# Performance work log

Measured on AMD Instinct MI355X. Metric: run time of the kernel, lower is better.

The kernel has to match this reference:

```python
import jax, jax.numpy as jnp
import numpy as np

WZ, WH, WW = 2, 6, 12
WIN = WZ * WH * WW  # 144
DEPTH, DIM, HEADS = 2, 192, 6
NEG = -1e9


def earth_position_index():
    zi = np.arange(WZ); zj = -np.arange(WZ) * WZ
    hi = np.arange(WH); hj = -np.arange(WH) * WH
    w = np.arange(WW)
    c1 = np.stack(np.meshgrid(zi, hi, w, indexing='ij')).reshape(3, -1)
    c2 = np.stack(np.meshgrid(zj, hj, w, indexing='ij')).reshape(3, -1)
    coords = (c1[:, :, None] - c2[:, None, :]).transpose(1, 2, 0).copy()
    coords[:, :, 2] += WW - 1
    coords[:, :, 1] *= 2 * WW - 1
    coords[:, :, 0] *= (2 * WW - 1) * WH * WH
    return jnp.asarray(coords.sum(-1))


def shift_mask(Z, H):
    # Swin-style mask over Z (vertical) and H (latitude); W (longitude) is circular.
    sz, sh = WZ // 2, WH // 2
    region = np.zeros((Z, H), np.int32)
    cnt = 0
    for zs in (slice(0, Z - WZ), slice(Z - WZ, Z - sz), slice(Z - sz, Z)):
        for hs in (slice(0, H - WH), slice(H - WH, H - sh), slice(H - sh, H)):
            region[zs, hs] = cnt; cnt += 1
    r = region.reshape(Z // WZ, WZ, H // WH, WH).transpose(0, 2, 1, 3).reshape(-1, WZ * WH)
    r = np.repeat(r, WW, axis=1)  # window token order is (z,h,w)
    m = np.where(r[:, :, None] == r[:, None, :], 0.0, NEG).astype(np.float32)
    return jnp.asarray(m)


def window_partition(x, Z, H, W):
    B, C = x.shape[0], x.shape[-1]
    x = x.reshape(B, Z // WZ, WZ, H // WH, WH, W // WW, WW, C)
    x = x.transpose(0, 1, 3, 5, 2, 4, 6, 7)
    return x.reshape(B, (Z // WZ) * (H // WH) * (W // WW), WIN, C)


def window_reverse(xw, Z, H, W):
    B, C = xw.shape[0], xw.shape[-1]
    x = xw.reshape(B, Z // WZ, H // WH, W // WW, WZ, WH, WW, C)
    x = x.transpose(0, 1, 4, 2, 5, 3, 6, 7)
    return x.reshape(B, Z, H, W, C)


def layernorm(x, g, b):
    mu = x.mean(-1, keepdims=True)
    var = jnp.mean((x - mu) ** 2, axis=-1, keepdims=True)
    return (x - mu) * jax.lax.rsqrt(var + 1e-5) * g + b


def attn_windows(xw, qkv_w, qkv_b, proj_w, proj_b, bias_tab, pos_idx, mask):
    B, nW, N, C = xw.shape
    hd = C // HEADS
    qkv = (xw @ qkv_w + qkv_b).reshape(B, nW, N, 3, HEADS, hd)
    q, k, v = qkv[..., 0, :, :], qkv[..., 1, :, :], qkv[..., 2, :, :]
    attn = jnp.einsum('bwnhd,bwmhd->bwhnm', q * (hd ** -0.5), k)
    bias = bias_tab[pos_idx]
    attn = attn + bias.transpose(2, 0, 1)[None, None]
    if mask is not None:
        nzh = mask.shape[0]
        attn = attn.reshape(B, nzh, nW // nzh, HEADS, N, N) + mask[None, :, None, None]
        attn = attn.reshape(B, nW, HEADS, N, N)
    attn = jax.nn.softmax(attn, axis=-1)
    out = jnp.einsum('bwhnm,bwmhd->bwnhd', attn, v).reshape(B, nW, N, C)
    return out @ proj_w + proj_b


def forward(x, qkv_w, qkv_b, proj_w, proj_b, bias_tab,
            ln1_g, ln1_b, ln2_g, ln2_b, mlp_w1, mlp_b1, mlp_w2, mlp_b2, Z, H, W):
    B, L, C = x.shape
    pos_idx = earth_position_index()
    mask = shift_mask(Z, H)
    depth = qkv_w.shape[0]
    for i in range(depth):
        roll = (i % 2 == 1)
        shortcut = x
        xg = x.reshape(B, Z, H, W, C)
        if roll:
            xg = jnp.roll(xg, (-(WZ // 2), -(WH // 2), -(WW // 2)), axis=(1, 2, 3))
        xw = window_partition(xg, Z, H, W)
        xw = attn_windows(xw, qkv_w[i], qkv_b[i], proj_w[i], proj_b[i],
                          bias_tab[i], pos_idx, mask if roll else None)
        xg = window_reverse(xw, Z, H, W)
        if roll:
            xg = jnp.roll(xg, (WZ // 2, WH // 2, WW // 2), axis=(1, 2, 3))
        xa = xg.reshape(B, L, C)
        x = shortcut + layernorm(xa, ln1_g[i], ln1_b[i])
        h = jax.nn.gelu(x @ mlp_w1[i] + mlp_b1[i], approximate=False)
        h = h @ mlp_w2[i] + mlp_b2[i]
        x = x + layernorm(h, ln2_g[i], ln2_b[i])
    return x


def setup_inputs() -> dict:
    key = jax.random.key(0)
    ks = jax.random.split(key, 16)
    B, Z, H, W, C = 1, 8, 96, 180, DIM
    L = Z * H * W
    bias_rows = (2 * WW - 1) * WH * WH * WZ * WZ  # 3312
    s = 0.02
    return {
        'x': jax.random.normal(ks[0], (B, L, C), jnp.float32),
        'qkv_w': jax.random.normal(ks[1], (DEPTH, C, 3 * C), jnp.float32) * s,
        'qkv_b': jnp.zeros((DEPTH, 3 * C), jnp.float32),
        'proj_w': jax.random.normal(ks[2], (DEPTH, C, C), jnp.float32) * s,
        'proj_b': jnp.zeros((DEPTH, C), jnp.float32),
        'bias_tab': jax.random.normal(ks[3], (DEPTH, bias_rows, HEADS), jnp.float32) * s,
        'ln1_g': jnp.ones((DEPTH, C), jnp.float32),
        'ln1_b': jnp.zeros((DEPTH, C), jnp.float32),
        'ln2_g': jnp.ones((DEPTH, C), jnp.float32),
        'ln2_b': jnp.zeros((DEPTH, C), jnp.float32),
        'mlp_w1': jax.random.normal(ks[4], (DEPTH, C, 4 * C), jnp.float32) * s,
        'mlp_b1': jnp.zeros((DEPTH, 4 * C), jnp.float32),
        'mlp_w2': jax.random.normal(ks[5], (DEPTH, 4 * C, C), jnp.float32) * s,
        'mlp_b2': jnp.zeros((DEPTH, C), jnp.float32),
        'Z': Z, 'H': H, 'W': W,
    }


def reference(x, qkv_w, qkv_b, proj_w, proj_b, bias_tab, ln1_g, ln1_b, ln2_g, ln2_b,
              mlp_w1, mlp_b1, mlp_w2, mlp_b2, Z, H, W):
    return forward(x, qkv_w, qkv_b, proj_w, proj_b, bias_tab, ln1_g, ln1_b,
                   ln2_g, ln2_b, mlp_w1, mlp_b1, mlp_w2, mlp_b2, Z, H, W)
```

## Files before the change

kernel.cpp:

```cpp
#include <hip/hip_runtime.h>
#include <hip/hip_bf16.h>
#include <math.h>

#define L_TOK 138240
#define NW 960

typedef __attribute__((ext_vector_type(8))) short s16x8;
typedef __attribute__((ext_vector_type(8))) unsigned short u16x8;
typedef __attribute__((ext_vector_type(4))) unsigned short u16x4;
typedef __attribute__((ext_vector_type(4))) float f32x4;

__device__ __forceinline__ float bf2f(unsigned short u){
  union{unsigned int u;float f;} v; v.u=((unsigned int)u)<<16; return v.f;
}
__device__ __forceinline__ unsigned short f2bf(float f){
  __hip_bfloat16 b = __float2bfloat16(f);
  union { __hip_bfloat16 b; unsigned short u; } v; v.b = b; return v.u;
}
__device__ __forceinline__ void gll16(const void* g, void* l) {
  __builtin_amdgcn_global_load_lds((const __attribute__((address_space(1))) void*)g,
                                   (__attribute__((address_space(3))) void*)l, 16, 0, 0);
}
__device__ __forceinline__ float gelu_f(float v){
  const float s = v * 0.70710678118654752f;
  const float a = fabsf(s);
  const float t = 1.0f / (1.0f + 0.3275911f * a);
  float p = 1.061405429f;
  p = p*t - 1.453152027f;
  p = p*t + 1.421413741f;
  p = p*t - 0.284496736f;
  p = p*t + 0.254829592f;
  p = p*t;
  float y = 1.0f - p * __expf(-a*a);
  y = copysignf(y, s);
  return 0.5f * v * (1.0f + y);
}

template<int NTILES>
__global__ __launch_bounds__(256) void gemm_qkv(
    const unsigned short* __restrict__ xb,
    const unsigned short* __restrict__ Bt,
    const float* __restrict__ bias,
    unsigned short* __restrict__ out)
{
  __shared__ unsigned short As[64*192];
  const int tid = threadIdx.x;
  const int wid = tid >> 6, lane = tid & 63;
  const int lr = lane & 15, kg = lane >> 4;
  const int bm = blockIdx.x;
  const int wn = wid * 16;
  const int N = NTILES * 64;

  #pragma unroll
  for (int i = 0; i < 6; i++) {
    const int c = tid + i*256;
    const int r = c / 24, s = c % 24;
    const int sg = (s & 24) | ((s ^ r) & 7);
    gll16(&xb[(size_t)(bm*64 + r)*192 + sg*8], &As[c*8]);
  }
  __syncthreads();

  s16x8 a[4][6];
  #pragma unroll
  for (int mi = 0; mi < 4; mi++)
    #pragma unroll
    for (int ks = 0; ks < 6; ks++) {
      const int m = mi*16 + lr, g = ks*4 + kg;
      const int sg = (g & 24) | ((g ^ m) & 7);
      a[mi][ks] = *(const s16x8*)&As[m*192 + sg*8];
    }

  for (int bn = 0; bn < NTILES; bn++) {
    s16x8 b[6];
    #pragma unroll
    for (int ks = 0; ks < 6; ks++)
      b[ks] = *(const s16x8*)&Bt[(size_t)(bn*64 + wn + lr)*192 + ks*32 + kg*8];
    f32x4 acc[4] = {};
    #pragma unroll
    for (int ks = 0; ks < 6; ks++)
      #pragma unroll
      for (int mi = 0; mi < 4; mi++)
        acc[mi] = __builtin_amdgcn_mfma_f32_16x16x32_bf16(a[mi][ks], b[ks], acc[mi], 0, 0, 0);
    const int col = bn*64 + wn + lr;
    const float bv = bias[col];
    #pragma unroll
    for (int mi = 0; mi < 4; mi++)
      #pragma unroll
      for (int q = 0; q < 4; q++) {
        const int row = bm*64 + mi*16 + kg*4 + q;
        out[(size_t)row*N + col] = f2bf(acc[mi][q] + bv);
      }
  }
}

__global__ __launch_bounds__(256) void gemm_ln(
    const unsigned short* __restrict__ A,
    const unsigned short* __restrict__ Bt,
    const float* __restrict__ bias, const float* __restrict__ g,
    const float* __restrict__ bta,
    unsigned short* __restrict__ xbo,
    int lda)
{
  __shared__ unsigned short As[2][128*32];
  __shared__ unsigned short Bs[2][192*32];
  __shared__ float rowstat[128][2][2];
  const int tid = threadIdx.x;
  const int wid = tid >> 6, lane = tid & 63;
  const int lr = lane & 15, kg = lane >> 4;
  const int bm = blockIdx.x;
  const int wm = (wid >> 1) * 64, wn = (wid & 1) * 96;
  const int rsub = lane >> 2, kc = lane & 3;
  const int K = 192;

  f32x4 acc[4][6] = {};
  const int nst = K / 32;

  #pragma unroll
  for (int i = 0; i < 2; i++)
    gll16(&A[(size_t)(bm*128 + wid*32 + i*16 + rsub)*lda + kc*8], &As[0][(wid*32 + i*16)*32]);
  #pragma unroll
  for (int j = 0; j < 3; j++)
    gll16(&Bt[(size_t)(wid*48 + j*16 + rsub)*K + kc*8], &Bs[0][(wid*48 + j*16)*32]);
  __syncthreads();

  for (int t = 0; t < nst; t++) {
    const int cur = t & 1, nxt = cur ^ 1;
    if (t + 1 < nst) {
      const int k1 = (t+1)*32;
      #pragma unroll
      for (int i = 0; i < 2; i++)
        gll16(&A[(size_t)(bm*128 + wid*32 + i*16 + rsub)*lda + k1 + kc*8], &As[nxt][(wid*32 + i*16)*32]);
      #pragma unroll
      for (int j = 0; j < 3; j++)
        gll16(&Bt[(size_t)(wid*48 + j*16 + rsub)*K + k1 + kc*8], &Bs[nxt][(wid*48 + j*16)*32]);
    }
    s16x8 a[4], b[6];
    #pragma unroll
    for (int mi = 0; mi < 4; mi++) a[mi] = *(const s16x8*)&As[cur][(wm + mi*16 + lr)*32 + kg*8];
    #pragma unroll
    for (int ni = 0; ni < 6; ni++) b[ni] = *(const s16x8*)&Bs[cur][(wn + ni*16 + lr)*32 + kg*8];
    #pragma unroll
    for (int mi = 0; mi < 4; mi++)
      #pragma unroll
      for (int ni = 0; ni < 6; ni++)
        acc[mi][ni] = __builtin_amdgcn_mfma_f32_16x16x32_bf16(a[mi], b[ni], acc[mi][ni], 0, 0, 0);
    __syncthreads();
  }

  float bv[6], gv[6], btv[6];
  #pragma unroll
  for (int ni = 0; ni < 6; ni++) {
    const int col = wn + ni*16 + lr;
    bv[ni] = bias[col]; gv[ni] = g[col]; btv[ni] = bta[col];
  }
  #pragma unroll
  for (int mi = 0; mi < 4; mi++) {
    float s[4] = {0,0,0,0}, ss[4] = {0,0,0,0};
    #pragma unroll
    for (int ni = 0; ni < 6; ni++)
      #pragma unroll
      for (int q = 0; q < 4; q++) {
        const float v = acc[mi][ni][q] + bv[ni];
        s[q] += v; ss[q] += v*v;
      }
    #pragma unroll
    for (int q = 0; q < 4; q++) {
      #pragma unroll
      for (int m = 1; m < 16; m <<= 1) {
        s[q]  += __shfl_xor(s[q],  m, 64);
        ss[q] += __shfl_xor(ss[q], m, 64);
      }
    }
    if (lr == 0) {
      #pragma unroll
      for (int q = 0; q < 4; q++) {
        const int r = wm + mi*16 + kg*4 + q;
        rowstat[r][wid & 1][0] = s[q];
        rowstat[r][wid & 1][1] = ss[q];
      }
    }
  }
  __syncthreads();
  #pragma unroll
  for (int mi = 0; mi < 4; mi++) {
    #pragma unroll
    for (int q = 0; q < 4; q++) {
      const int rl = wm + mi*16 + kg*4 + q;
      const float s  = rowstat[rl][0][0] + rowstat[rl][1][0];
      const float ss = rowstat[rl][0][1] + rowstat[rl][1][1];
      const float mu = s * (1.0f/192.0f);
      const float rs = rsqrtf(ss * (1.0f/192.0f) - mu*mu + 1e-5f);
      const size_t grow = (size_t)(bm*128 + rl) * 192;
      #pragma unroll
      for (int ni = 0; ni < 6; ni++) {
        const float v = acc[mi][ni][q] + bv[ni];
        const float o = (v - mu) * rs * gv[ni] + btv[ni];
        const size_t idx = grow + wn + ni*16 + lr;
        xbo[idx] = f2bf(bf2f(xbo[idx]) + o);
      }
    }
  }
}

template<int WF32>
__global__ __launch_bounds__(256) void fused_mlp(
    const unsigned short* __restrict__ xb,
    const unsigned short* __restrict__ W1t,
    const unsigned short* __restrict__ W2t,
    const float* __restrict__ b1, const float* __restrict__ b2,
    const float* __restrict__ g, const float* __restrict__ bt,
    unsigned short* __restrict__ xbo, float* __restrict__ xf)
{
  __shared__ unsigned short As[64*192];
  __shared__ unsigned short Hs[64*64];
  __shared__ float rowstat[64][4][2];
  const int tid = threadIdx.x, wid = tid >> 6, lane = tid & 63;
  const int lr = lane & 15, kg = lane >> 4;
  const int row0 = blockIdx.x * 64;

  #pragma unroll
  for (int i = 0; i < 6; i++) {
    const int c = tid + i*256;
    const int r = c / 24, s = c % 24;
    const int sg = (s & 24) | ((s ^ r) & 7);
    gll16(&xb[(size_t)(row0 + r)*192 + sg*8], &As[c*8]);
  }
  __syncthreads();

  char* const hs = (char*)&Hs[0];

  f32x4 yacc[4][3] = {};
  for (int t = 0; t < 12; t++) {
    s16x8 w1f[6];
    #pragma unroll
    for (int ks = 0; ks < 6; ks++)
      w1f[ks] = *(const s16x8*)&W1t[(size_t)(t*64 + wid*16 + lr)*192 + ks*32 + kg*8];
    const float4 b1q = *(const float4*)&b1[t*64 + wid*16 + kg*4];
    u16x4 hv[4];
    #pragma unroll
    for (int mb = 0; mb < 4; mb++) {
      const int m = mb*16 + lr;
      f32x4 hacc = {0.f, 0.f, 0.f, 0.f};
      #pragma unroll
      for (int ks = 0; ks < 6; ks++) {
        const int gsl = ks*4 + kg;
        const int sg = (gsl & 24) | ((gsl ^ m) & 7);
        const s16x8 xf8 = *(const s16x8*)&As[m*192 + sg*8];
        hacc = __builtin_amdgcn_mfma_f32_16x16x32_bf16(w1f[ks], xf8, hacc, 0, 0, 0);
      }
      hv[mb][0] = f2bf(gelu_f(hacc[0] + b1q.x));
      hv[mb][1] = f2bf(gelu_f(hacc[1] + b1q.y));
      hv[mb][2] = f2bf(gelu_f(hacc[2] + b1q.z));
      hv[mb][3] = f2bf(gelu_f(hacc[3] + b1q.w));
    }
    __syncthreads();
    {
      const int cb = wid*32 + kg*8;
      #pragma unroll
      for (int mb = 0; mb < 4; mb++) {
        const int m = mb*16 + lr;
        *(u16x4*)(hs + m*128 + (cb ^ ((m & 7) << 4))) = hv[mb];
      }
    }
    __syncthreads();
    #pragma unroll
    for (int kk = 0; kk < 2; kk++) {
      s16x8 b2f[3];
      #pragma unroll
      for (int nj = 0; nj < 3; nj++)
        b2f[nj] = *(const s16x8*)&W2t[(size_t)(wid*48 + nj*16 + lr)*768 + t*64 + kk*32 + kg*8];
      #pragma unroll
      for (int mi = 0; mi < 4; mi++) {
        const int m = mi*16 + lr;
        const int cb2 = kk*64 + kg*16;
        const s16x8 a2 = *(const s16x8*)(hs + m*128 + (cb2 ^ ((m & 7) << 4)));
        #pragma unroll
        for (int nj = 0; nj < 3; nj++)
          yacc[mi][nj] = __builtin_amdgcn_mfma_f32_16x16x32_bf16(a2, b2f[nj], yacc[mi][nj], 0, 0, 0);
      }
    }
  }

  float bv[3], gv[3], btv[3];
  #pragma unroll
  for (int nj = 0; nj < 3; nj++) {
    const int col = wid*48 + nj*16 + lr;
    bv[nj] = b2[col]; gv[nj] = g[col]; btv[nj] = bt[col];
  }
  #pragma unroll
  for (int mi = 0; mi < 4; mi++) {
    float s[4] = {0,0,0,0}, ss[4] = {0,0,0,0};
    #pragma unroll
    for (int nj = 0; nj < 3; nj++)
      #pragma unroll
      for (int q = 0; q < 4; q++) {
        const float v = yacc[mi][nj][q] + bv[nj];
        s[q] += v; ss[q] += v*v;
      }
    #pragma unroll
    for (int q = 0; q < 4; q++) {
      #pragma unroll
      for (int m = 1; m < 16; m <<= 1) {
        s[q]  += __shfl_xor(s[q],  m, 64);
        ss[q] += __shfl_xor(ss[q], m, 64);
      }
    }
    if (lr == 0) {
      #pragma unroll
      for (int q = 0; q < 4; q++) {
        rowstat[mi*16 + kg*4 + q][wid][0] = s[q];
        rowstat[mi*16 + kg*4 + q][wid][1] = ss[q];
      }
    }
  }
  __syncthreads();
  #pragma unroll
  for (int mi = 0; mi < 4; mi++) {
    #pragma unroll
    for (int q = 0; q < 4; q++) {
      const int rl = mi*16 + kg*4 + q;
      const float s  = rowstat[rl][0][0] + rowstat[rl][1][0] + rowstat[rl][2][0] + rowstat[rl][3][0];
      const float ss = rowstat[rl][0][1] + rowstat[rl][1][1] + rowstat[rl][2][1] + rowstat[rl][3][1];
      const float mu = s * (1.0f/192.0f);
      const float rs = rsqrtf(ss * (1.0f/192.0f) - mu*mu + 1e-5f);
      const size_t grow = (size_t)(row0 + rl) * 192;
      #pragma unroll
      for (int nj = 0; nj < 3; nj++) {
        const float v = yacc[mi][nj][q] + bv[nj];
        const float o = (v - mu) * rs * gv[nj] + btv[nj];
        const size_t idx = grow + wid*48 + nj*16 + lr;
        const float xn = bf2f(xbo[idx]) + o;
        xbo[idx] = f2bf(xn);
        if (WF32) xf[idx] = xn;
      }
    }
  }
}

__global__ __launch_bounds__(384) void attn_win7(
    unsigned short* qkv,
    const unsigned short* __restrict__ biasbt,
    int roll)
{
  __shared__ unsigned short Pw[6][16][168];
  __shared__ int lmap[144];

  const int w = blockIdx.x;
  const int tid = threadIdx.x, wid = tid / 64, lane = tid & 63;
  const int lr = lane & 15, kg = lane >> 4;
  const int ww = w % 15, hw = (w / 15) % 16, zw = w / 240;

  if (tid < 144) {
    const int z1 = tid / 72, h1 = (tid % 72) / 12, w1 = tid % 12;
    int z = zw*2 + z1, h = hw*6 + h1, xx = ww*12 + w1;
    if (roll) { z = (z + 1) & 7; h = (h + 3) % 96; xx = (xx + 6) % 180; }
    lmap[tid] = (z*96 + h)*180 + xx;
  }
  __syncthreads();

  const unsigned short* bb;
  if (roll) {
    const int c = ((zw == 3) ? 2 : 0) | ((hw == 15) ? 1 : 0);
    bb = biasbt + (size_t)c*124416 + (size_t)wid*20736;
  } else {
    bb = biasbt + (size_t)wid*20736;
  }

  s16x8 kfr[9];
  #pragma unroll
  for (int ti = 0; ti < 9; ti++)
    kfr[ti] = *(const s16x8*)&qkv[(size_t)lmap[ti*16 + lr]*576 + 192 + wid*32 + kg*8];

  s16x8 vbr[2][5];
  #pragma unroll
  for (int ci = 0; ci < 2; ci++)
    #pragma unroll
    for (int ks = 0; ks < 5; ks++) {
      u16x8 t;
      #pragma unroll
      for (int j = 0; j < 8; j++) {
        const int tok = ks*32 + kg*8 + j;
        t[j] = (tok < 144) ? qkv[(size_t)lmap[tok]*576 + 384 + wid*32 + ci*16 + lr] : (unsigned short)0;
      }
      vbr[ci][ks] = (s16x8)t;
    }

  #pragma unroll
  for (int j = 0; j < 4; j++) Pw[wid][lr][144 + kg*4 + j] = 0;

  for (int s = 0; s < 9; s++) {
    const s16x8 bq = *(const s16x8*)&qkv[(size_t)lmap[s*16 + lr]*576 + wid*32 + kg*8];

    float pb[9][4];
    float mx = -3.0e38f;
    #pragma unroll
    for (int ti = 0; ti < 9; ti++) {
      f32x4 acc = {0.f, 0.f, 0.f, 0.f};
      acc = __builtin_amdgcn_mfma_f32_16x16x32_bf16(kfr[ti], bq, acc, 0, 0, 0);
      const u16x4 b4 = *(const u16x4*)&bb[(size_t)(s*9 + ti)*256 + lr*16 + kg*4];
      #pragma unroll
      for (int q = 0; q < 4; q++) {
        const float sv = acc[q] + bf2f(b4[q]);
        pb[ti][q] = sv;
        mx = fmaxf(mx, sv);
      }
    }
    mx = fmaxf(mx, __shfl_xor(mx, 16, 64));
    mx = fmaxf(mx, __shfl_xor(mx, 32, 64));

    float sum = 0.f;
    #pragma unroll
    for (int ti = 0; ti < 9; ti++)
      #pragma unroll
      for (int q = 0; q < 4; q++) {
        const float p = __expf(pb[ti][q] - mx);
        pb[ti][q] = p;
        sum += p;
      }
    sum += __shfl_xor(sum, 16, 64);
    sum += __shfl_xor(sum, 32, 64);
    const float inv = 1.0f / sum;

    #pragma unroll
    for (int ti = 0; ti < 9; ti++)
      #pragma unroll
      for (int q = 0; q < 4; q++)
        Pw[wid][lr][ti*16 + kg*4 + q] = f2bf(pb[ti][q] * inv);

    #pragma unroll
    for (int ci = 0; ci < 2; ci++) {
      f32x4 accO = {0.f, 0.f, 0.f, 0.f};
      #pragma unroll
      for (int ks = 0; ks < 5; ks++) {
        const s16x8 pa = *(const s16x8*)&Pw[wid][lr][ks*32 + kg*8];
        accO = __builtin_amdgcn_mfma_f32_16x16x32_bf16(pa, vbr[ci][ks], accO, 0, 0, 0);
      }
      #pragma unroll
      for (int q = 0; q < 4; q++) {
        const int row = s*16 + kg*4 + q;
        qkv[(size_t)lmap[row]*576 + wid*32 + ci*16 + lr] = f2bf(accO[q]);
      }
    }
  }
}

__global__ void init_xb(const float* __restrict__ xin, unsigned short* __restrict__ xb, int n) {
  const int i = blockIdx.x*256 + threadIdx.x;
  if (i < n) xb[i] = f2bf(xin[i]);
}
__global__ void copy_diag(const float* __restrict__ a, float* __restrict__ o, int n) {
  const int i = blockIdx.x*256 + threadIdx.x;
  if (i < n) o[i] = a[i] + 50.0f;
}
__global__ void transpose_w(const float* __restrict__ src, unsigned short* __restrict__ dst,
                            int K, int N, int nscale, float factor) {
  const int i = blockIdx.x*256 + threadIdx.x;
  const int tot = K*N;
  if (i >= 2*tot) return;
  const int l = i / tot, e = i % tot;
  const int k = e / N, n = e % N;
  float v = src[i];
  if (n < nscale) v *= factor;
  dst[(size_t)l*tot + (size_t)n*K + k] = f2bf(v);
}
__global__ void scale_qb(const float* __restrict__ src, float* __restrict__ dst) {
  const int i = blockIdx.x*256 + threadIdx.x;
  if (i >= 2*576) return;
  const float f = (i % 576) < 192 ? 0.17677669529663687f : 1.0f;
  dst[i] = src[i] * f;
}
__global__ void build_biasb6(const float* __restrict__ tab, unsigned short* __restrict__ bm) {
  const int i = blockIdx.x*256 + threadIdx.x;
  const int TAB = 6*144*144;
  if (i >= 5*TAB) return;
  const int tau = i / TAB, r = i % TAB;
  const int hd = r / 20736, rr = r % 20736;
  const int s = rr / 2304, rrr = rr % 2304;
  const int ti = rrr / 256, e = rrr % 256;
  const int lr_ = e / 16, c4 = e % 16;
  const int q = s*16 + lr_, tok = ti*16 + c4;
  const int z1 = q/72,  h1 = (q%72)/12,  w1 = q%12;
  const int z2 = tok/72, h2 = (tok%72)/12, w2 = tok%12;
  const int idx = (z1 + 2*z2)*828 + (h1 + 6*h2)*23 + (w1 - w2 + 11);
  const int l = (tau == 0) ? 0 : 1;
  float v = tab[(size_t)l*3312*6 + (size_t)idx*6 + hd];
  if (tau >= 1) {
    const int c = tau - 1, zs = c >> 1, hs = c & 1;
    const int rq = (zs ? (1 + z1) : 0)*3 + (hs ? (1 + (h1 >= 3)) : 0);
    const int rt = (zs ? (1 + z2) : 0)*3 + (hs ? (1 + (h2 >= 3)) : 0);
    if (rq != rt) v -= 1.0e9f;
  }
  bm[i] = f2bf(v);
}

extern "C" void kernel_launch(void* const* d_in, const int* in_sizes, int n_in,
                              void* d_out, int out_size, void* d_ws, size_t ws_size,
                              hipStream_t stream) {
  const float* x_in    = (const float*)d_in[0];
  const float* qkv_w   = (const float*)d_in[1];
  const float* qkv_b   = (const float*)d_in[2];
  const float* proj_w  = (const float*)d_in[3];
  const float* proj_b  = (const float*)d_in[4];
  const float* bias_tab= (const float*)d_in[5];
  const float* ln1_g   = (const float*)d_in[6];
  const float* ln1_b   = (const float*)d_in[7];
  const float* ln2_g   = (const float*)d_in[8];
  const float* ln2_b   = (const float*)d_in[9];
  const float* mlp_w1  = (const float*)d_in[10];
  const float* mlp_b1  = (const float*)d_in[11];
  const float* mlp_w2  = (const float*)d_in[12];
  const float* mlp_b2  = (const float*)d_in[13];

  const int nElem = L_TOK * 192;
  float* xf = (float*)d_out;

  const size_t sz_R0 = 159252480;
  const size_t sz_xb = 53084160;
  const size_t sz_wT = 1769472;
  const size_t sz_bb = 2488320;
  const size_t sz_qb = 4608;
  const size_t need  = sz_R0 + sz_xb + sz_wT + sz_bb + sz_qb;

  if (ws_size < need) {
    copy_diag<<<dim3((nElem+255)/256), 256, 0, stream>>>(x_in, xf, nElem);
    return;
  }

  char* ws = (char*)d_ws;
  unsigned short* R0    = (unsigned short*)(ws);
  unsigned short* xb    = (unsigned short*)(ws + sz_R0);
  unsigned short* wT    = (unsigned short*)(ws + sz_R0 + sz_xb);
  unsigned short* biasb = (unsigned short*)(ws + sz_R0 + sz_xb + sz_wT);
  float*          qb2   = (float*)(ws + sz_R0 + sz_xb + sz_wT + sz_bb);

  unsigned short* wT_qkv  = wT;
  unsigned short* wT_proj = wT + 221184;
  unsigned short* wT_m1   = wT + 294912;
  unsigned short* wT_m2   = wT + 589824;

  transpose_w<<<dim3((2*192*576+255)/256), 256, 0, stream>>>(qkv_w,  wT_qkv, 192, 576, 192, 0.17677669529663687f);
  transpose_w<<<dim3((2*192*192+255)/256), 256, 0, stream>>>(proj_w, wT_proj,192, 192, 0, 1.0f);
  transpose_w<<<dim3((2*192*768+255)/256), 256, 0, stream>>>(mlp_w1, wT_m1,  192, 768, 0, 1.0f);
  transpose_w<<<dim3((2*768*192+255)/256), 256, 0, stream>>>(mlp_w2, wT_m2,  768, 192, 0, 1.0f);
  build_biasb6<<<dim3((5*6*144*144+255)/256), 256, 0, stream>>>(bias_tab, biasb);
  scale_qb<<<dim3(5), 256, 0, stream>>>(qkv_b, qb2);

  init_xb<<<dim3((nElem+255)/256), 256, 0, stream>>>(x_in, xb, nElem);

  for (int i = 0; i < 2; i++) {
    gemm_qkv<9><<<dim3(2160), 256, 0, stream>>>(
        xb, wT_qkv + (size_t)i*110592, qb2 + i*576, R0);
    attn_win7<<<dim3(NW), 384, 0, stream>>>(
        R0, biasb + (i ? 124416 : 0), i & 1);
    gemm_ln<<<dim3(1080), 256, 0, stream>>>(
        R0, wT_proj + (size_t)i*36864, proj_b + i*192,
        ln1_g + i*192, ln1_b + i*192, xb, 576);
    if (i == 0)
      fused_mlp<0><<<dim3(2160), 256, 0, stream>>>(
          xb, wT_m1, wT_m2, mlp_b1, mlp_b2,
          ln2_g, ln2_b, xb, nullptr);
    else
      fused_mlp<1><<<dim3(2160), 256, 0, stream>>>(
          xb, wT_m1 + (size_t)147456, wT_m2 + (size_t)147456,
          mlp_b1 + 768, mlp_b2 + 192,
          ln2_g + 192, ln2_b + 192, xb, xf);
  }
}
```

Measured before the change: 937.9 us.

## Double-buffer MLP hidden tile and prefetch next W1 fragments in fused_mlp

The fused MLP kernel now keeps two LDS buffers for the GELU hidden tile, which removes one of the two barriers per hidden-chunk iteration. It prefetches the next chunk's W1 fragments into registers during the second GEMM, and issues the W2 fragment loads before the GELU epilogue. The goal is to overlap global weight loads with MFMA work and cut sync stalls. In exchange, register pressure and LDS usage go up (an extra 8 KB), which may lower occupancy.

```diff
diff --git a/kernel.cpp b/kernel.cpp
--- a/kernel.cpp
+++ b/kernel.cpp
@@ -212,7 +212,7 @@
     unsigned short* __restrict__ xbo, float* __restrict__ xf)
 {
   __shared__ unsigned short As[64*192];
-  __shared__ unsigned short Hs[64*64];
+  __shared__ unsigned short Hs[2][64*64];
   __shared__ float rowstat[64][4][2];
   const int tid = threadIdx.x, wid = tid >> 6, lane = tid & 63;
   const int lr = lane & 15, kg = lane >> 4;
@@ -227,56 +227,67 @@
   }
   __syncthreads();
 
-  char* const hs = (char*)&Hs[0];
+  char* const hs0 = (char*)&Hs[0][0];
+  char* const hs1 = (char*)&Hs[1][0];
 
   f32x4 yacc[4][3] = {};
+  s16x8 w1f[6];
+  #pragma unroll
+  for (int ks = 0; ks < 6; ks++)
+    w1f[ks] = *(const s16x8*)&W1t[(size_t)(wid*16 + lr)*192 + ks*32 + kg*8];
+
   for (int t = 0; t < 12; t++) {
-    s16x8 w1f[6];
-    #pragma unroll
-    for (int ks = 0; ks < 6; ks++)
-      w1f[ks] = *(const s16x8*)&W1t[(size_t)(t*64 + wid*16 + lr)*192 + ks*32 + kg*8];
-    const float4 b1q = *(const float4*)&b1[t*64 + wid*16 + kg*4];
-    u16x4 hv[4];
+    char* const hb = (t & 1) ? hs1 : hs0;
+    f32x4 hacc[4];
     #pragma unroll
     for (int mb = 0; mb < 4; mb++) {
       const int m = mb*16 + lr;
-      f32x4 hacc = {0.f, 0.f, 0.f, 0.f};
+      hacc[mb] = f32x4{0.f, 0.f, 0.f, 0.f};
       #pragma unroll
       for (int ks = 0; ks < 6; ks++) {
         const int gsl = ks*4 + kg;
         const int sg = (gsl & 24) | ((gsl ^ m) & 7);
         const s16x8 xf8 = *(const s16x8*)&As[m*192 + sg*8];
-        hacc = __builtin_amdgcn_mfma_f32_16x16x32_bf16(w1f[ks], xf8, hacc, 0, 0, 0);
-      }
-      hv[mb][0] = f2bf(gelu_f(hacc[0] + b1q.x));
-      hv[mb][1] = f2bf(gelu_f(hacc[1] + b1q.y));
-      hv[mb][2] = f2bf(gelu_f(hacc[2] + b1q.z));
-      hv[mb][3] = f2bf(gelu_f(hacc[3] + b1q.w));
-    }
-    __syncthreads();
+        hacc[mb] = __builtin_amdgcn_mfma_f32_16x16x32_bf16(w1f[ks], xf8, hacc[mb], 0, 0, 0);
+      }
+    }
+    s16x8 b2f[6];
+    #pragma unroll
+    for (int kk = 0; kk < 2; kk++)
+      #pragma unroll
+      for (int nj = 0; nj < 3; nj++)
+        b2f[kk*3 + nj] = *(const s16x8*)&W2t[(size_t)(wid*48 + nj*16 + lr)*768 + t*64 + kk*32 + kg*8];
+
+    const float4 b1q = *(const float4*)&b1[t*64 + wid*16 + kg*4];
     {
       const int cb = wid*32 + kg*8;
       #pragma unroll
       for (int mb = 0; mb < 4; mb++) {
         const int m = mb*16 + lr;
-        *(u16x4*)(hs + m*128 + (cb ^ ((m & 7) << 4))) = hv[mb];
+        u16x4 hv;
+        hv[0] = f2bf(gelu_f(hacc[mb][0] + b1q.x));
+        hv[1] = f2bf(gelu_f(hacc[mb][1] + b1q.y));
+        hv[2] = f2bf(gelu_f(hacc[mb][2] + b1q.z));
+        hv[3] = f2bf(gelu_f(hacc[mb][3] + b1q.w));
+        *(u16x4*)(hb + m*128 + (cb ^ ((m & 7) << 4))) = hv;
       }
     }
     __syncthreads();
+    if (t < 11) {
+      #pragma unroll
+      for (int ks = 0; ks < 6; ks++)
+        w1f[ks] = *(const s16x8*)&W1t[(size_t)((t+1)*64 + wid*16 + lr)*192 + ks*32 + kg*8];
+    }
     #pragma unroll
     for (int kk = 0; kk < 2; kk++) {
-      s16x8 b2f[3];
-      #pragma unroll
-      for (int nj = 0; nj < 3; nj++)
-        b2f[nj] = *(const s16x8*)&W2t[(size_t)(wid*48 + nj*16 + lr)*768 + t*64 + kk*32 + kg*8];
       #pragma unroll
       for (int mi = 0; mi < 4; mi++) {
         const int m = mi*16 + lr;
         const int cb2 = kk*64 + kg*16;
-        const s16x8 a2 = *(const s16x8*)(hs + m*128 + (cb2 ^ ((m & 7) << 4)));
+        const s16x8 a2 = *(const s16x8*)(hb + m*128 + (cb2 ^ ((m & 7) << 4)));
         #pragma unroll
         for (int nj = 0; nj < 3; nj++)
-          yacc[mi][nj] = __builtin_amdgcn_mfma_f32_16x16x32_bf16(a2, b2f[nj], yacc[mi][nj], 0, 0, 0);
+          yacc[mi][nj] = __builtin_amdgcn_mfma_f32_16x16x32_bf16(a2, b2f[kk*3 + nj], yacc[mi][nj], 0, 0, 0);
       }
     }
   }
```

After: 881.4 us, median of 4. 6.0% less time.
